# Kernel optimization log

Hardware: AMD Instinct MI355X
Metric: run time of the kernel (lower is better)

Reference implementation:

```python
import jax, jax.numpy as jnp
import numpy as np


def lstm_cell(x, h, c, wih, whh, bih, bhh):
    # torch gate order: i, f, g, o
    g = x @ wih.T + bih + h @ whh.T + bhh
    i, f, gg, o = jnp.split(g, 4, axis=-1)
    c = jax.nn.sigmoid(f) * c + jax.nn.sigmoid(i) * jnp.tanh(gg)
    h = jax.nn.sigmoid(o) * jnp.tanh(c)
    return h, c


def lstm_layer(xs, h0, c0, wih, whh, bih, bhh):
    # xs: [T, B, in]
    def step(carry, x_t):
        h, c = lstm_cell(x_t, carry[0], carry[1], wih, whh, bih, bhh)
        return (h, c), h
    (h, c), hs = jax.lax.scan(step, (h0, c0), xs)
    return hs, h, c


def setup_inputs() -> dict:
    key = jax.random.key(0)
    B, T, H, IN = 256, 512, 512, 1
    ks = jax.random.split(key, 32)
    r = lambda k, shape: (jax.random.normal(k, shape, dtype=jnp.float32) * 0.05)
    inp = {
        "x": jax.random.normal(ks[0], (B, T, IN), dtype=jnp.float32),
        "future": 64,
        # main LSTM (2 layers)
        "w_ih0": r(ks[1], (4 * H, IN)), "w_hh0": r(ks[2], (4 * H, H)),
        "b_ih0": r(ks[3], (4 * H,)),   "b_hh0": r(ks[4], (4 * H,)),
        "w_ih1": r(ks[5], (4 * H, H)), "w_hh1": r(ks[6], (4 * H, H)),
        "b_ih1": r(ks[7], (4 * H,)),   "b_hh1": r(ks[8], (4 * H,)),
        "fc_w": r(ks[9], (1, H)),      "fc_b": r(ks[10], (1,)),
        # prediction LSTM (2 layers) + its head
        "pw_ih0": r(ks[11], (4 * H, 1)), "pw_hh0": r(ks[12], (4 * H, H)),
        "pb_ih0": r(ks[13], (4 * H,)),   "pb_hh0": r(ks[14], (4 * H,)),
        "pw_ih1": r(ks[15], (4 * H, H)), "pw_hh1": r(ks[16], (4 * H, H)),
        "pb_ih1": r(ks[17], (4 * H,)),   "pb_hh1": r(ks[18], (4 * H,)),
        "pfc_w": r(ks[19], (1, H)),      "pfc_b": r(ks[20], (1,)),
    }
    return inp


def reference(x, future, w_ih0, w_hh0, b_ih0, b_hh0, w_ih1, w_hh1, b_ih1, b_hh1,
              fc_w, fc_b, pw_ih0, pw_hh0, pb_ih0, pb_hh0, pw_ih1, pw_hh1,
              pb_ih1, pb_hh1, pfc_w, pfc_b):
    B = x.shape[0]
    H = w_hh0.shape[1]
    z = jnp.zeros((B, H), dtype=jnp.float32)
    xs = jnp.swapaxes(x, 0, 1)  # [T, B, 1]
    # warmup pass over the observed sequence (inference: dropout inactive)
    hs0, h0, c0 = lstm_layer(xs, z, z, w_ih0, w_hh0, b_ih0, b_hh0)
    hs1, h1, c1 = lstm_layer(hs0, z, z, w_ih1, w_hh1, b_ih1, b_hh1)
    out = hs1[-1] @ fc_w.T + fc_b  # [B, 1]

    def pstep(carry, _):
        o, h0, c0, h1, c1 = carry
        h0, c0 = lstm_cell(o, h0, c0, pw_ih0, pw_hh0, pb_ih0, pb_hh0)
        h1, c1 = lstm_cell(h0, h1, c1, pw_ih1, pw_hh1, pb_ih1, pb_hh1)
        o = h1 @ pfc_w.T + pfc_b
        return (o, h0, c0, h1, c1), o

    _, outs = jax.lax.scan(pstep, (out, h0, c0, h1, c1), None, length=future - 1)
    all_outs = jnp.concatenate([out[None], outs], axis=0)  # [future, B, 1]
    return jnp.swapaxes(all_outs[..., 0], 0, 1)  # [B, future]
```

## Files before the change

### kernel.cpp

```cpp
#include <hip/hip_runtime.h>
#include <hip/hip_bf16.h>

#define TT  512
#define BB  256
#define HH  512
#define FUT 64
#define NBLK 128


struct Hdr { int dtflag; };

typedef __attribute__((ext_vector_type(8))) short short8;
typedef __attribute__((ext_vector_type(4))) float floatx4;

#define OFF_CTR   4096
#define OFF_W     8192
#define WSZ       ((size_t)2048*512*2)
#define OFF_H     (OFF_W + 6*WSZ)
#define HSZ       ((size_t)BB*HH*2)
#define OFF_OA    (OFF_H + 4*HSZ)
#define OASZ      ((size_t)FUT*BB*4)
#define NEED_WS   (OFF_OA + OASZ)

#define SPIN_CAP  (1L << 24)

__device__ __forceinline__ float bf2f(short s) {
  unsigned u = ((unsigned)(unsigned short)s) << 16;
  return __builtin_bit_cast(float, u);
}
__device__ __forceinline__ short f2bf(float f) {
  unsigned u = __builtin_bit_cast(unsigned, f);
  u = u + 0x7FFFu + ((u >> 16) & 1u);
  return (short)(u >> 16);
}
__device__ __forceinline__ float ldf(const void* p, long i, int dt) {
  return dt ? ((const float*)p)[i] : bf2f(((const short*)p)[i]);
}
__device__ __forceinline__ short8 cohld16(const short* p) {
  short8 v;
  asm volatile("global_load_dwordx4 %0, %1, off sc0 sc1"
               : "=v"(v) : "v"(p));
  return v;
}
__device__ __forceinline__ void cohst16(short* p, short8 v) {
  asm volatile("global_store_dwordx4 %0, %1, off sc0 sc1"
               :: "v"(p), "v"(v) : "memory");
}
#define WAITV(N) do { asm volatile("s_waitcnt vmcnt(" #N ")" ::: "memory"); \
                      __builtin_amdgcn_sched_barrier(0); } while (0)

__global__ void beacon_kernel(float* dout, float v) {
  if (threadIdx.x == 0) dout[0] = v;
}

__global__ __launch_bounds__(256) void probe1_kernel(const void* w, Hdr* hdr) {
  const int tid = threadIdx.x;
  const short* s = (const short*)w;
  float mx = 0.f;
  #pragma unroll
  for (int i = 0; i < 16; ++i) {
    float v = fabsf(bf2f(s[tid * 16 + i]));
    if (!(v == v)) v = 1e30f;
    mx = fmaxf(mx, v);
  }
  #pragma unroll
  for (int off = 32; off > 0; off >>= 1) mx = fmaxf(mx, __shfl_down(mx, off));
  __shared__ float wmax[4];
  if ((tid & 63) == 0) wmax[tid >> 6] = mx;
  __syncthreads();
  if (tid == 0) {
    float m = fmaxf(fmaxf(wmax[0], wmax[1]), fmaxf(wmax[2], wmax[3]));
    hdr->dtflag = (m > 1000.f) ? 1 : 0;
  }
}

__global__ __launch_bounds__(256) void cvt_kernel(const void* src, short* dst,
                                                  const Hdr* hdr) {
  const int dt = hdr->dtflag;
  const long i = ((long)blockIdx.x * 256 + threadIdx.x);
  if (dt) {
    const float4 v = ((const float4*)src)[i];
    short4 o;
    o.x = f2bf(v.x); o.y = f2bf(v.y); o.z = f2bf(v.z); o.w = f2bf(v.w);
    ((short4*)dst)[i] = o;
  } else {
    ((short4*)dst)[i] = ((const short4*)src)[i];
  }
}

__global__ __launch_bounds__(512, 1) void lstm_persist(
    const void* __restrict__ x,
    const void* __restrict__ w_ih0, const void* __restrict__ b_ih0,
    const void* __restrict__ b_hh0, const void* __restrict__ b_ih1,
    const void* __restrict__ b_hh1, const void* __restrict__ fc_w,
    const void* __restrict__ fc_b,  const void* __restrict__ pw_ih0,
    const void* __restrict__ pb_ih0, const void* __restrict__ pb_hh0,
    const void* __restrict__ pb_ih1, const void* __restrict__ pb_hh1,
    const void* __restrict__ pfc_w, const void* __restrict__ pfc_b,
    const short* __restrict__ Whh0, const short* __restrict__ Wih1,
    const short* __restrict__ Whh1, const short* __restrict__ pWhh0,
    const short* __restrict__ pWih1, const short* __restrict__ pWhh1,
    short* H0a, short* H0b, short* H1a, short* H1b,
    float* oA, int* ctr, const Hdr* __restrict__ hdr,
    float* __restrict__ dout)
{
  const int dt  = hdr->dtflag;
  const int tid = threadIdx.x;
  const int role = blockIdx.x & 1;
  const int bg   = (blockIdx.x >> 1) & 1;
  const int ug   = blockIdx.x >> 2;
  const int U0   = ug * 16;
  const int B0   = bg * 128;
  int* grpArr = ctr + 32 + (blockIdx.x >> 4) * 32;
  int* grpRel = ctr + 32 + (blockIdx.x >> 4) * 32 + 16;
  const int isMaster = (blockIdx.x & 15) == 0;

  __shared__ __align__(16) short Wl[2][64][64][8];
  __shared__ __align__(16) short hbuf[128][16];
  __shared__ float bs[64];
  __shared__ float wih[64];

  const int lane = tid & 63;
  const int wv   = tid >> 6;
  const int ln   = lane & 15;
  const int q    = lane >> 4;
  const int bl   = wv*16 + ln;
  const long abase = (long)(B0 + bl) * 512 + q*8;

  float cst[4] = {0.f, 0.f, 0.f, 0.f};
  float fwk[4] = {0.f, 0.f, 0.f, 0.f};

  short *h0c = H0a, *h0n = H0b, *h1c = H1a, *h1n = H1b;
  int ph = 0;

#define STAGE16(SLOT, WG)                                                    \
  for (int i = tid; i < 4096; i += 512) {                                    \
    const int ks_ = i & 63, r_ = i >> 6;                                     \
    const long gr = (long)((r_ & 3) * 512 + U0 + (r_ >> 2)) * 512 + ks_ * 8; \
    *(short8*)&Wl[SLOT][ks_][r_][0] = *(const short8*)((WG) + gr);           \
  }

#define BIAS16(B1, B2, WIHP)                                                 \
  if (tid < 64) {                                                            \
    const long j = (long)(tid & 3) * 512 + U0 + (tid >> 2);                  \
    bs[tid] = ldf((B1), j, dt) + ldf((B2), j, dt);                           \
    wih[tid] = (WIHP) ? ldf((const void*)(WIHP), j, dt) : 0.f;               \
  }

#define FWLOAD(FWP)                                                          \
  { _Pragma("unroll")                                                        \
    for (int mt = 0; mt < 4; ++mt)                                           \
      fwk[mt] = ldf((FWP), U0 + mt*4 + q, dt); }

#define ZACC(A)                                                              \
  _Pragma("unroll") for (int mt_ = 0; mt_ < 4; ++mt_)                        \
    A[mt_] = (floatx4){0.f, 0.f, 0.f, 0.f};

#define GSEG1N(AP, ACC)                                                      \
  { const short* ap_ = (AP) + abase;                                         \
    short8 abuf[2][8];                                                       \
    _Pragma("unroll")                                                        \
    for (int i = 0; i < 8; ++i) abuf[0][i] = cohld16(ap_ + i*32);            \
    _Pragma("unroll")                                                        \
    for (int g = 0; g < 2; ++g) {                                            \
      if (g == 0) {                                                          \
        _Pragma("unroll")                                                    \
        for (int i = 0; i < 8; ++i)                                          \
          abuf[1][i] = cohld16(ap_ + (8+i)*32);                              \
        WAITV(8);                                                            \
      } else { WAITV(0); }                                                   \
      _Pragma("unroll")                                                      \
      for (int kk = 0; kk < 8; ++kk) {                                       \
        const int kb = g*8 + kk;                                             \
        _Pragma("unroll")                                                    \
        for (int mt = 0; mt < 4; ++mt) {                                     \
          short8 wf = *(const short8*)&Wl[0][kb*4 + q][mt*16 + ln][0];       \
          ACC[mt] = __builtin_amdgcn_mfma_f32_16x16x32_bf16(                 \
              wf, abuf[g][kk], ACC[mt], 0, 0, 0);                            \
        }                                                                    \
      }                                                                      \
    } }

#define GSEG2N(AP0, AP1, ACC)                                                \
  { const short* p0_ = (AP0) + abase;                                        \
    const short* p1_ = (AP1) + abase;                                        \
    short8 abuf[2][8];                                                       \
    _Pragma("unroll")                                                        \
    for (int i = 0; i < 8; ++i) abuf[0][i] = cohld16(p0_ + i*32);            \
    _Pragma("unroll")                                                        \
    for (int g = 0; g < 4; ++g) {                                            \
      if (g < 3) {                                                           \
        const short* np_ = ((g+1)&1) ? p1_ : p0_;                            \
        const int nb_ = ((g+1)>>1)*8;                                        \
        _Pragma("unroll")                                                    \
        for (int i = 0; i < 8; ++i)                                          \
          abuf[(g+1)&1][i] = cohld16(np_ + (nb_+i)*32);                      \
        WAITV(8);                                                            \
      } else { WAITV(0); }                                                   \
      const int sg_ = g & 1;                                                 \
      const int kbb_ = (g >> 1) * 8;                                         \
      _Pragma("unroll")                                                      \
      for (int kk = 0; kk < 8; ++kk) {                                       \
        const int kb = kbb_ + kk;                                            \
        _Pragma("unroll")                                                    \
        for (int mt = 0; mt < 4; ++mt) {                                     \
          short8 wf = *(const short8*)&Wl[sg_][kb*4 + q][mt*16 + ln][0];     \
          ACC[mt] = __builtin_amdgcn_mfma_f32_16x16x32_bf16(                 \
              wf, abuf[g&1][kk], ACC[mt], 0, 0, 0);                          \
        }                                                                    \
      }                                                                      \
    } }

#define EPI16(ACC, MODE, TV, SVO, HOUT, OSLOT)                               \
  { float sv = 0.f;                                                          \
    if ((MODE) == 0)      sv = ldf(x, (long)(B0 + bl)*TT + (TV), dt);        \
    else if ((MODE) == 2) sv = (SVO);                                        \
    float po = 0.f;                                                          \
    _Pragma("unroll")                                                        \
    for (int mt = 0; mt < 4; ++mt) {                                         \
      const int u = mt*4 + q;                                                \
      float gi = ACC[mt][0] + bs[u*4+0];                                     \
      float gf = ACC[mt][1] + bs[u*4+1];                                     \
      float gg = ACC[mt][2] + bs[u*4+2];                                     \
      float go = ACC[mt][3] + bs[u*4+3];                                     \
      if ((MODE) != 1) {                                                     \
        gi += sv*wih[u*4+0]; gf += sv*wih[u*4+1];                            \
        gg += sv*wih[u*4+2]; go += sv*wih[u*4+3];                            \
      }                                                                      \
      const float I = 1.f/(1.f+expf(-gi));                                   \
      const float F = 1.f/(1.f+expf(-gf));                                   \
      const float G = tanhf(gg);                                             \
      const float O = 1.f/(1.f+expf(-go));                                   \
      const float cn = F*cst[mt] + I*G;                                      \
      cst[mt] = cn;                                                          \
      const short hb16 = f2bf(O * tanhf(cn));                                \
      hbuf[bl][u] = hb16;                                                    \
      if ((OSLOT) != (float*)0) po += fwk[mt] * bf2f(hb16);                  \
    }                                                                        \
    if ((OSLOT) != (float*)0) {                                              \
      po += __shfl_xor(po, 16); po += __shfl_xor(po, 32);                    \
      if (lane < 16) atomicAdd((float*)(OSLOT) + bl, po);                    \
    }                                                                        \
    __syncthreads();                                                         \
    if (tid < 256) {                                                         \
      const int b_ = tid >> 1, hf_ = tid & 1;                                \
      short8 hv8 = *(const short8*)&hbuf[b_][hf_*8];                         \
      cohst16((HOUT) + (long)(B0 + b_)*512 + U0 + hf_*8, hv8);               \
    }                                                                        \
    asm volatile("s_waitcnt vmcnt(0)" ::: "memory"); }

#define SPIN(COND)                                                           \
  { long guard_ = 0;                                                         \
    while (COND) {                                                           \
      __builtin_amdgcn_s_sleep(1);                                           \
      if (++guard_ > SPIN_CAP) break;                                        \
    } }

#define GBAR()                                                               \
  { __syncthreads();                                                         \
    ++ph;                                                                    \
    if (tid == 0) {                                                          \
      asm volatile("s_waitcnt vmcnt(0)" ::: "memory");                       \
      __hip_atomic_fetch_add(grpArr, 1, __ATOMIC_RELAXED,                    \
                             __HIP_MEMORY_SCOPE_SYSTEM);                     \
      if (isMaster) {                                                        \
        SPIN(__hip_atomic_load(grpArr, __ATOMIC_RELAXED,                     \
                               __HIP_MEMORY_SCOPE_SYSTEM) < ph * 16);        \
        __hip_atomic_fetch_add(ctr, 1, __ATOMIC_RELAXED,                     \
                               __HIP_MEMORY_SCOPE_SYSTEM);                   \
        SPIN(__hip_atomic_load(ctr, __ATOMIC_RELAXED,                        \
                               __HIP_MEMORY_SCOPE_SYSTEM) < ph * 8);         \
        __hip_atomic_store(grpRel, ph, __ATOMIC_RELAXED,                     \
                           __HIP_MEMORY_SCOPE_SYSTEM);                       \
      } else {                                                               \
        SPIN(__hip_atomic_load(grpRel, __ATOMIC_RELAXED,                     \
                               __HIP_MEMORY_SCOPE_SYSTEM) < ph);             \
      }                                                                      \
    }                                                                        \
    __syncthreads(); }

  if (role == 0) {
    STAGE16(0, Whh0);
    BIAS16(b_ih0, b_hh0, w_ih0);
  } else {
    STAGE16(0, Wih1); STAGE16(1, Whh1);
    BIAS16(b_ih1, b_hh1, (const void*)0);
    FWLOAD(fc_w);
  }
  const float fcb  = ldf(fc_b, 0, dt);
  const float pfcb = ldf(pfc_b, 0, dt);
  __syncthreads();

  for (int t = 0; t < TT; ++t) {
    if (role == 0) {
      floatx4 a[4]; ZACC(a);
      GSEG1N(h0c, a);
      EPI16(a, 0, t, 0.f, h0n, (float*)0);
    } else if (t > 0) {
      floatx4 a[4]; ZACC(a);
      GSEG2N(h0c, h1c, a);
      EPI16(a, 1, 0, 0.f, h1n, (float*)0);
    }
    GBAR();
    { short* t_ = h0c; h0c = h0n; h0n = t_; }
    if (t > 0) { short* t_ = h1c; h1c = h1n; h1n = t_; }
  }
  if (role == 1) {
    floatx4 a[4]; ZACC(a);
    GSEG2N(h0c, h1c, a);
    EPI16(a, 1, 0, 0.f, h1n, oA + B0);
  }
  GBAR();
  { short* t_ = h1c; h1c = h1n; h1n = t_; }

  if (role == 0) {
    STAGE16(0, pWhh0);
    BIAS16(pb_ih0, pb_hh0, pw_ih0);
  } else {
    STAGE16(0, pWih1); STAGE16(1, pWhh1);
    BIAS16(pb_ih1, pb_hh1, (const void*)0);
    FWLOAD(pfc_w);
  }
  __syncthreads();

  for (int s = 1; s < FUT; ++s) {
    if (role == 0) {
      const float ob_ = (s == 1) ? fcb : pfcb;
      const float o_ = __hip_atomic_load(
          oA + (long)(s-1)*BB + B0 + bl,
          __ATOMIC_RELAXED, __HIP_MEMORY_SCOPE_SYSTEM) + ob_;
      if (ug == 0 && lane < 16)
        dout[(long)(B0 + bl)*FUT + (s-1)] = o_;
      floatx4 a[4]; ZACC(a);
      GSEG1N(h0c, a);
      EPI16(a, 2, 0, o_, h0n, (float*)0);
    }
    GBAR();
    { short* t_ = h0c; h0c = h0n; h0n = t_; }
    if (role == 1) {
      floatx4 a[4]; ZACC(a);
      GSEG2N(h0c, h1c, a);
      EPI16(a, 1, 0, 0.f, h1n, oA + (long)s*BB + B0);
    }
    GBAR();
    { short* t_ = h1c; h1c = h1n; h1n = t_; }
  }
  if (role == 0 && ug == 0 && lane < 16) {
    const float o_ = __hip_atomic_load(
        oA + (long)(FUT-1)*BB + B0 + bl,
        __ATOMIC_RELAXED, __HIP_MEMORY_SCOPE_SYSTEM) + pfcb;
    dout[(long)(B0 + bl)*FUT + (FUT-1)] = o_;
  }
#undef STAGE16
#undef BIAS16
#undef FWLOAD
#undef ZACC
#undef GSEG1N
#undef GSEG2N
#undef EPI16
#undef SPIN
#undef GBAR
}

extern "C" void kernel_launch(void* const* d_in, const int* in_sizes, int n_in,
                              void* d_out, int out_size, void* d_ws, size_t ws_size,
                              hipStream_t stream) {
  float* dout = (float*)d_out;

  static const int exp_sizes[22] = {
    131072, 1, 2048, 1048576, 2048, 2048, 1048576, 1048576, 2048, 2048,
    512, 1, 2048, 1048576, 2048, 2048, 1048576, 1048576, 2048, 2048, 512, 1};
  int code = -1, m = 0;
  if (n_in != 22) { code = 0; m = n_in & 127; }
  else {
    for (int i = 0; i < 22; ++i)
      if (in_sizes[i] != exp_sizes[i]) { code = 1; m = i; break; }
  }
  if (code < 0 && out_size != BB * FUT) { code = 6; m = (out_size >> 8) & 127; }
  if (code < 0 && (d_ws == nullptr || ws_size < NEED_WS)) {
    code = 2; m = (int)(ws_size >> 20); if (m > 127) m = 127;
  }
  if (code >= 0) {
    float v = ldexpf(1.f + (float)m / 128.f, 20 + code);
    beacon_kernel<<<dim3(1), dim3(64), 0, stream>>>(dout, v);
    return;
  }

  const void* x      = d_in[0];
  const void* w_ih0  = d_in[2];
  const void* w_hh0  = d_in[3];
  const void* b_ih0  = d_in[4];
  const void* b_hh0  = d_in[5];
  const void* w_ih1  = d_in[6];
  const void* w_hh1  = d_in[7];
  const void* b_ih1  = d_in[8];
  const void* b_hh1  = d_in[9];
  const void* fc_w   = d_in[10];
  const void* fc_b   = d_in[11];
  const void* pw_ih0 = d_in[12];
  const void* pw_hh0 = d_in[13];
  const void* pb_ih0 = d_in[14];
  const void* pb_hh0 = d_in[15];
  const void* pw_ih1 = d_in[16];
  const void* pw_hh1 = d_in[17];
  const void* pb_ih1 = d_in[18];
  const void* pb_hh1 = d_in[19];
  const void* pfc_w  = d_in[20];
  const void* pfc_b  = d_in[21];

  char* ws = (char*)d_ws;
  Hdr* hdr = (Hdr*)ws;
  int* ctr = (int*)(ws + OFF_CTR);
  short* Wc[6];
  for (int i = 0; i < 6; ++i) Wc[i] = (short*)(ws + OFF_W + (size_t)i*WSZ);
  short* H0a = (short*)(ws + OFF_H);
  short* H0b = (short*)(ws + OFF_H + HSZ);
  short* H1a = (short*)(ws + OFF_H + 2*HSZ);
  short* H1b = (short*)(ws + OFF_H + 3*HSZ);
  float* oA  = (float*)(ws + OFF_OA);

  hipMemsetAsync(ws, 0, 8192, stream);
  hipMemsetAsync(H0a, 0, HSZ, stream);
  hipMemsetAsync(H1a, 0, HSZ, stream);
  hipMemsetAsync(oA, 0, OASZ, stream);
  probe1_kernel<<<dim3(1), dim3(256), 0, stream>>>(w_hh0, hdr);

  dim3 cg(1024), cb(256);
  cvt_kernel<<<cg, cb, 0, stream>>>(w_hh0,  Wc[0], hdr);
  cvt_kernel<<<cg, cb, 0, stream>>>(w_ih1,  Wc[1], hdr);
  cvt_kernel<<<cg, cb, 0, stream>>>(w_hh1,  Wc[2], hdr);
  cvt_kernel<<<cg, cb, 0, stream>>>(pw_hh0, Wc[3], hdr);
  cvt_kernel<<<cg, cb, 0, stream>>>(pw_ih1, Wc[4], hdr);
  cvt_kernel<<<cg, cb, 0, stream>>>(pw_hh1, Wc[5], hdr);

  lstm_persist<<<dim3(NBLK), dim3(512), 0, stream>>>(
      x, w_ih0, b_ih0, b_hh0, b_ih1, b_hh1, fc_w, fc_b,
      pw_ih0, pb_ih0, pb_hh0, pb_ih1, pb_hh1, pfc_w, pfc_b,
      Wc[0], Wc[1], Wc[2], Wc[3], Wc[4], Wc[5],
      H0a, H0b, H1a, H1b, oA, ctr, hdr, dout);
}
```

Baseline: 7.208 ms.

## Replace global barriers with per-step producer/consumer flags and ring-buffered hidden states

Swaps the two-level grid-wide barrier for per-timestep counter flags per batch group, so layer-0 blocks can run ahead of layer-1 blocks. Layer 0 is wavefronted against layer 1, with a 4-slot ring for h0 and a 2-slot ring for h1. Consumption counters stop slots from being overwritten before they are read. This is meant to remove full-grid barrier latency and the serialisation between the two layers each step. In exchange it adds more polling on many flags, uses more workspace, and risks subtle ordering bugs under relaxed atomics.

```diff
diff --git a/kernel.cpp b/kernel.cpp
--- a/kernel.cpp
+++ b/kernel.cpp
@@ -13,16 +13,17 @@
 typedef __attribute__((ext_vector_type(8))) short short8;
 typedef __attribute__((ext_vector_type(4))) float floatx4;
 
-#define OFF_CTR   4096
-#define OFF_W     8192
+#define OFF_FLG   4096
+#define OFF_W     20480
 #define WSZ       ((size_t)2048*512*2)
-#define OFF_H     (OFF_W + 6*WSZ)
+#define OFF_H0    (OFF_W + 6*WSZ)
 #define HSZ       ((size_t)BB*HH*2)
-#define OFF_OA    (OFF_H + 4*HSZ)
+#define OFF_H1    (OFF_H0 + 4*HSZ)
+#define OFF_OA    (OFF_H1 + 2*HSZ)
 #define OASZ      ((size_t)FUT*BB*4)
 #define NEED_WS   (OFF_OA + OASZ)
 
-#define SPIN_CAP  (1L << 24)
+#define SPIN_CAP  (1L << 22)
 
 __device__ __forceinline__ float bf2f(short s) {
   unsigned u = ((unsigned)(unsigned short)s) << 16;
@@ -100,9 +101,8 @@
     const short* __restrict__ Whh0, const short* __restrict__ Wih1,
     const short* __restrict__ Whh1, const short* __restrict__ pWhh0,
     const short* __restrict__ pWih1, const short* __restrict__ pWhh1,
-    short* H0a, short* H0b, short* H1a, short* H1b,
-    float* oA, int* ctr, const Hdr* __restrict__ hdr,
-    float* __restrict__ dout)
+    short* H0R, short* H1R, float* oA, int* flg,
+    const Hdr* __restrict__ hdr, float* __restrict__ dout)
 {
   const int dt  = hdr->dtflag;
   const int tid = threadIdx.x;
@@ -111,9 +111,12 @@
   const int ug   = blockIdx.x >> 2;
   const int U0   = ug * 16;
   const int B0   = bg * 128;
-  int* grpArr = ctr + 32 + (blockIdx.x >> 4) * 32;
-  int* grpRel = ctr + 32 + (blockIdx.x >> 4) * 32 + 16;
-  const int isMaster = (blockIdx.x & 15) == 0;
+
+  int* F     = flg + bg * 2048;
+  int* pub0  = F;
+  int* pub1  = F + 576;
+  int* cons1 = F + 1152;
+  int* opub  = F + 1728;
 
   __shared__ __align__(16) short Wl[2][64][64][8];
   __shared__ __align__(16) short hbuf[128][16];
@@ -130,8 +133,21 @@
   float cst[4] = {0.f, 0.f, 0.f, 0.f};
   float fwk[4] = {0.f, 0.f, 0.f, 0.f};
 
-  short *h0c = H0a, *h0n = H0b, *h1c = H1a, *h1n = H1b;
-  int ph = 0;
+#define H0S(G) (H0R + (size_t)((G) & 3) * 131072)
+#define H1S(G) (H1R + (size_t)((G) & 1) * 131072)
+
+#define SPIN(COND)                                                           \
+  { long guard_ = 0;                                                         \
+    while (COND) {                                                           \
+      __builtin_amdgcn_s_sleep(1);                                           \
+      if (++guard_ > SPIN_CAP) break;                                        \
+    } }
+#define POLL(P, T)                                                           \
+  SPIN(__hip_atomic_load((P), __ATOMIC_RELAXED,                              \
+                         __HIP_MEMORY_SCOPE_SYSTEM) < (T))
+#define FADD(P)                                                              \
+  __hip_atomic_fetch_add((P), 1, __ATOMIC_RELAXED,                           \
+                         __HIP_MEMORY_SCOPE_SYSTEM)
 
 #define STAGE16(SLOT, WG)                                                    \
   for (int i = tid; i < 4096; i += 512) {                                    \
@@ -247,36 +263,7 @@
       short8 hv8 = *(const short8*)&hbuf[b_][hf_*8];                         \
       cohst16((HOUT) + (long)(B0 + b_)*512 + U0 + hf_*8, hv8);               \
     }                                                                        \
-    asm volatile("s_waitcnt vmcnt(0)" ::: "memory"); }
-
-#define SPIN(COND)                                                           \
-  { long guard_ = 0;                                                         \
-    while (COND) {                                                           \
-      __builtin_amdgcn_s_sleep(1);                                           \
-      if (++guard_ > SPIN_CAP) break;                                        \
-    } }
-
-#define GBAR()                                                               \
-  { __syncthreads();                                                         \
-    ++ph;                                                                    \
-    if (tid == 0) {                                                          \
-      asm volatile("s_waitcnt vmcnt(0)" ::: "memory");                       \
-      __hip_atomic_fetch_add(grpArr, 1, __ATOMIC_RELAXED,                    \
-                             __HIP_MEMORY_SCOPE_SYSTEM);                     \
-      if (isMaster) {                                                        \
-        SPIN(__hip_atomic_load(grpArr, __ATOMIC_RELAXED,                     \
-                               __HIP_MEMORY_SCOPE_SYSTEM) < ph * 16);        \
-        __hip_atomic_fetch_add(ctr, 1, __ATOMIC_RELAXED,                     \
-                               __HIP_MEMORY_SCOPE_SYSTEM);                   \
-        SPIN(__hip_atomic_load(ctr, __ATOMIC_RELAXED,                        \
-                               __HIP_MEMORY_SCOPE_SYSTEM) < ph * 8);         \
-        __hip_atomic_store(grpRel, ph, __ATOMIC_RELAXED,                     \
-                           __HIP_MEMORY_SCOPE_SYSTEM);                       \
-      } else {                                                               \
-        SPIN(__hip_atomic_load(grpRel, __ATOMIC_RELAXED,                     \
-                               __HIP_MEMORY_SCOPE_SYSTEM) < ph);             \
-      }                                                                      \
-    }                                                                        \
+    asm volatile("s_waitcnt vmcnt(0)" ::: "memory");                         \
     __syncthreads(); }
 
   if (role == 0) {
@@ -291,40 +278,29 @@
   const float pfcb = ldf(pfc_b, 0, dt);
   __syncthreads();
 
-  for (int t = 0; t < TT; ++t) {
-    if (role == 0) {
+  if (role == 0) {
+    for (int g = 0; g < TT; ++g) {
+      if (tid == 0) {
+        if (g > 0)  POLL(pub0 + g - 1, 32);
+        if (g >= 4) POLL(cons1 + g - 4, 32);
+      }
+      __syncthreads();
       floatx4 a[4]; ZACC(a);
-      GSEG1N(h0c, a);
-      EPI16(a, 0, t, 0.f, h0n, (float*)0);
-    } else if (t > 0) {
-      floatx4 a[4]; ZACC(a);
-      GSEG2N(h0c, h1c, a);
-      EPI16(a, 1, 0, 0.f, h1n, (float*)0);
+      GSEG1N(H0S(g-1), a);
+      EPI16(a, 0, g, 0.f, H0S(g), (float*)0);
+      if (tid == 0) FADD(pub0 + g);
     }
-    GBAR();
-    { short* t_ = h0c; h0c = h0n; h0n = t_; }
-    if (t > 0) { short* t_ = h1c; h1c = h1n; h1n = t_; }
-  }
-  if (role == 1) {
-    floatx4 a[4]; ZACC(a);
-    GSEG2N(h0c, h1c, a);
-    EPI16(a, 1, 0, 0.f, h1n, oA + B0);
-  }
-  GBAR();
-  { short* t_ = h1c; h1c = h1n; h1n = t_; }
-
-  if (role == 0) {
     STAGE16(0, pWhh0);
     BIAS16(pb_ih0, pb_hh0, pw_ih0);
-  } else {
-    STAGE16(0, pWih1); STAGE16(1, pWhh1);
-    BIAS16(pb_ih1, pb_hh1, (const void*)0);
-    FWLOAD(pfc_w);
-  }
-  __syncthreads();
-
-  for (int s = 1; s < FUT; ++s) {
-    if (role == 0) {
+    __syncthreads();
+    for (int s = 1; s < FUT; ++s) {
+      const int g = 511 + s;
+      if (tid == 0) {
+        POLL(pub0 + g - 1, 32);
+        POLL(cons1 + g - 4, 32);
+        POLL(opub + s - 1, 32);
+      }
+      __syncthreads();
       const float ob_ = (s == 1) ? fcb : pfcb;
       const float o_ = __hip_atomic_load(
           oA + (long)(s-1)*BB + B0 + bl,
@@ -332,24 +308,54 @@
       if (ug == 0 && lane < 16)
         dout[(long)(B0 + bl)*FUT + (s-1)] = o_;
       floatx4 a[4]; ZACC(a);
-      GSEG1N(h0c, a);
-      EPI16(a, 2, 0, o_, h0n, (float*)0);
+      GSEG1N(H0S(g-1), a);
+      EPI16(a, 2, 0, o_, H0S(g), (float*)0);
+      if (tid == 0) FADD(pub0 + g);
     }
-    GBAR();
-    { short* t_ = h0c; h0c = h0n; h0n = t_; }
-    if (role == 1) {
+    if (tid == 0) POLL(opub + FUT - 1, 32);
+    __syncthreads();
+    if (ug == 0 && lane < 16) {
+      const float o_ = __hip_atomic_load(
+          oA + (long)(FUT-1)*BB + B0 + bl,
+          __ATOMIC_RELAXED, __HIP_MEMORY_SCOPE_SYSTEM) + pfcb;
+      dout[(long)(B0 + bl)*FUT + (FUT-1)] = o_;
+    }
+  } else {
+    for (int g = 0; g < TT; ++g) {
+      if (tid == 0) {
+        POLL(pub0 + g, 32);
+        if (g > 0) POLL(pub1 + g - 1, 32);
+      }
+      __syncthreads();
       floatx4 a[4]; ZACC(a);
-      GSEG2N(h0c, h1c, a);
-      EPI16(a, 1, 0, 0.f, h1n, oA + (long)s*BB + B0);
+      GSEG2N(H0S(g), H1S(g-1), a);
+      __syncthreads();
+      if (tid == 0) FADD(cons1 + g);
+      float* os_ = (g == TT-1) ? (oA + B0) : (float*)0;
+      EPI16(a, 1, 0, 0.f, H1S(g), os_);
+      if (tid == 0) {
+        FADD(pub1 + g);
+        if (g == TT-1) FADD(opub + 0);
+      }
     }
-    GBAR();
-    { short* t_ = h1c; h1c = h1n; h1n = t_; }
-  }
-  if (role == 0 && ug == 0 && lane < 16) {
-    const float o_ = __hip_atomic_load(
-        oA + (long)(FUT-1)*BB + B0 + bl,
-        __ATOMIC_RELAXED, __HIP_MEMORY_SCOPE_SYSTEM) + pfcb;
-    dout[(long)(B0 + bl)*FUT + (FUT-1)] = o_;
+    STAGE16(0, pWih1); STAGE16(1, pWhh1);
+    BIAS16(pb_ih1, pb_hh1, (const void*)0);
+    FWLOAD(pfc_w);
+    __syncthreads();
+    for (int s = 1; s < FUT; ++s) {
+      const int g = 511 + s;
+      if (tid == 0) {
+        POLL(pub0 + g, 32);
+        POLL(pub1 + g - 1, 32);
+      }
+      __syncthreads();
+      floatx4 a[4]; ZACC(a);
+      GSEG2N(H0S(g), H1S(g-1), a);
+      __syncthreads();
+      if (tid == 0) FADD(cons1 + g);
+      EPI16(a, 1, 0, 0.f, H1S(g), oA + (long)s*BB + B0);
+      if (tid == 0) { FADD(pub1 + g); FADD(opub + s); }
+    }
   }
 #undef STAGE16
 #undef BIAS16
@@ -359,7 +365,10 @@
 #undef GSEG2N
 #undef EPI16
 #undef SPIN
-#undef GBAR
+#undef POLL
+#undef FADD
+#undef H0S
+#undef H1S
 }
 
 extern "C" void kernel_launch(void* const* d_in, const int* in_sizes, int n_in,
@@ -410,19 +419,15 @@
 
   char* ws = (char*)d_ws;
   Hdr* hdr = (Hdr*)ws;
-  int* ctr = (int*)(ws + OFF_CTR);
+  int* flg = (int*)(ws + OFF_FLG);
   short* Wc[6];
   for (int i = 0; i < 6; ++i) Wc[i] = (short*)(ws + OFF_W + (size_t)i*WSZ);
-  short* H0a = (short*)(ws + OFF_H);
-  short* H0b = (short*)(ws + OFF_H + HSZ);
-  short* H1a = (short*)(ws + OFF_H + 2*HSZ);
-  short* H1b = (short*)(ws + OFF_H + 3*HSZ);
+  short* H0R = (short*)(ws + OFF_H0);
+  short* H1R = (short*)(ws + OFF_H1);
   float* oA  = (float*)(ws + OFF_OA);
 
-  hipMemsetAsync(ws, 0, 8192, stream);
-  hipMemsetAsync(H0a, 0, HSZ, stream);
-  hipMemsetAsync(H1a, 0, HSZ, stream);
-  hipMemsetAsync(oA, 0, OASZ, stream);
+  hipMemsetAsync(ws, 0, 20480, stream);
+  hipMemsetAsync(H0R, 0, 4*HSZ + 2*HSZ + OASZ, stream);
   probe1_kernel<<<dim3(1), dim3(256), 0, stream>>>(w_hh0, hdr);
 
   dim3 cg(1024), cb(256);
@@ -437,5 +442,5 @@
       x, w_ih0, b_ih0, b_hh0, b_ih1, b_hh1, fc_w, fc_b,
       pw_ih0, pb_ih0, pb_hh0, pb_ih1, pb_hh1, pfc_w, pfc_b,
       Wc[0], Wc[1], Wc[2], Wc[3], Wc[4], Wc[5],
-      H0a, H0b, H1a, H1b, oA, ctr, hdr, dout);
-}
+      H0R, H1R, oA, flg, hdr, dout);
+}
```

Result: faster. 6.714 ms (-6.8%).
